# Optimization experiments

Measured on AMD Instinct MI355X. Metric: run time of the kernel, lower is better.

The kernel has to match this reference:

```python
import jax, jax.numpy as jnp
import numpy as np

B, S, D, H, O = 64, 512, 1024, 1024, 1024

def setup_inputs() -> dict:
    key = jax.random.key(0)
    k1, k2, k3 = jax.random.split(key, 3)
    x = jax.random.normal(k1, (B, S, D), dtype=jnp.float32)
    Wg = jax.random.normal(k2, (D + H, 3 * H), dtype=jnp.float32) / np.sqrt(D + H)
    bg = jnp.zeros((3 * H,), dtype=jnp.float32)
    Wc = jax.random.normal(k3, (H, O), dtype=jnp.float32) / np.sqrt(H)
    bc = jnp.zeros((O,), dtype=jnp.float32)
    return {"x": x, "Wg": Wg, "bg": bg, "Wc": Wc, "bc": bc}

def reference(x, Wg, bg, Wc, bc):
    # GRU cell matching the torch module: network = Linear(D+H, 3H)
    def step(h, x_t):
        combined = jnp.concatenate([x_t, h], axis=1)            # [B, D+H]
        gates = combined @ Wg + bg                              # [B, 3H]
        r_g, z_g, n_g = jnp.split(gates, 3, axis=1)
        r = jax.nn.sigmoid(r_g)
        z = jax.nn.sigmoid(z_g)
        n = jnp.tanh(n_g + r * h)
        h_next = (1 - z) * n + z * h
        return h_next, h_next

    h0 = jnp.zeros((x.shape[0], Wc.shape[0]), dtype=x.dtype)
    xs = jnp.swapaxes(x, 0, 1)                                  # [S, B, D]
    _, hs = jax.lax.scan(step, h0, xs)                          # hs: [S, B, H]
    outputs = jnp.swapaxes(hs, 0, 1)                            # [B, S, H]
    return outputs @ Wc + bc                                    # [B, S, O]
```

## Files before the change

### kernel.cpp

```cpp
#include <hip/hip_runtime.h>
#include <hip/hip_bf16.h>
#include <stdint.h>

#define BB   64
#define SS   512
#define DD   1024
#define HH   1024
#define TH3  3072
#define TCH  32

using frag8 = __attribute__((ext_vector_type(8))) short;
using f32x4 = __attribute__((ext_vector_type(4))) float;

__device__ __forceinline__ void split_bf16(float v, short& hi, short& lo) {
    uint32_t u = __float_as_uint(v);
    uint32_t uh = u & 0xFFFF0000u;
    float fl = v - __uint_as_float(uh);
    hi = (short)(uh >> 16);
    lo = (short)(__float_as_uint(fl) >> 16);
}

__global__ __launch_bounds__(256) void prep_w(
    const float* __restrict__ Wg, short* __restrict__ Wt_hi,
    short* __restrict__ Wt_lo)
{
    int idx = blockIdx.x * 256 + threadIdx.x;
    int lane = idx & 63;
    int f = idx >> 6;
    int kt = f & 63;
    int fg = f >> 6;
    int g = fg % 3;
    int jb = fg / 3;
    int krow = kt * 32 + (lane >> 4) * 8;
    int col = g * HH + jb * 16 + (lane & 15);
    size_t dst = (size_t)f * 512 + (size_t)lane * 8;
#pragma unroll
    for (int j = 0; j < 8; ++j) {
        float v = Wg[(size_t)(krow + j) * TH3 + col];
        short hi, lo;
        split_bf16(v, hi, lo);
        Wt_hi[dst + j] = hi;
        Wt_lo[dst + j] = lo;
    }
}

__global__ __launch_bounds__(256) void prep_wc(
    const float* __restrict__ Wc, short* __restrict__ Wct_hi,
    short* __restrict__ Wct_lo)
{
    int idx = blockIdx.x * 256 + threadIdx.x;
    int lane = idx & 63;
    int f = idx >> 6;
    int kt = f & 31;
    int jb = f >> 5;
    int krow = kt * 32 + (lane >> 4) * 8;
    int col = jb * 16 + (lane & 15);
    size_t dst = (size_t)f * 512 + (size_t)lane * 8;
#pragma unroll
    for (int j = 0; j < 8; ++j) {
        float v = Wc[(size_t)(krow + j) * HH + col];
        short hi, lo;
        split_bf16(v, hi, lo);
        Wct_hi[dst + j] = hi;
        Wct_lo[dst + j] = lo;
    }
}

__global__ __launch_bounds__(256) void gx_gemm(
    const short* __restrict__ Wt_hi, const short* __restrict__ Wt_lo,
    const float* __restrict__ x,
    const float* __restrict__ bg,
    float* __restrict__ gx,
    int t0)
{
    const int tid = threadIdx.x;
    const int lane = tid & 63;
    const int w = tid >> 6;
    const int jbg = blockIdx.x & 15;
    const int tl = blockIdx.x >> 4;
    const int t = t0 + tl;
    const int m0 = (w & 1) * 32;
    const int jbb = jbg * 4 + (w >> 1) * 2;
    const int kq = (lane >> 4) * 8;

    f32x4 acc[2][2][3];
#pragma unroll
    for (int mi = 0; mi < 2; ++mi)
#pragma unroll
        for (int jp = 0; jp < 2; ++jp)
#pragma unroll
            for (int g = 0; g < 3; ++g)
                acc[mi][jp][g] = (f32x4){0.f, 0.f, 0.f, 0.f};

    const float* xr0 = x + ((size_t)(m0 + (lane & 15)) * SS + t) * DD;
    const float* xr1 = xr0 + (size_t)16 * SS * DD;

    for (int kt = 0; kt < 32; ++kt) {
        frag8 ah[2], al[2];
#pragma unroll
        for (int mi = 0; mi < 2; ++mi) {
            const float* xp = (mi == 0 ? xr0 : xr1) + kt * 32 + kq;
            float xv[8];
            *(float4*)&xv[0] = *(const float4*)xp;
            *(float4*)&xv[4] = *(const float4*)(xp + 4);
#pragma unroll
            for (int j = 0; j < 8; ++j) {
                short hi, lo;
                split_bf16(xv[j], hi, lo);
                ah[mi][j] = hi;
                al[mi][j] = lo;
            }
        }
#pragma unroll
        for (int jp = 0; jp < 2; ++jp) {
#pragma unroll
            for (int g = 0; g < 3; ++g) {
                size_t base =
                    (((size_t)(jbb + jp) * 3 + g) * 64 + kt) * 512 + (size_t)lane * 8;
                frag8 bh = *(const frag8*)(Wt_hi + base);
                frag8 bl = *(const frag8*)(Wt_lo + base);
#pragma unroll
                for (int mi = 0; mi < 2; ++mi) {
                    f32x4 a = acc[mi][jp][g];
                    a = __builtin_amdgcn_mfma_f32_16x16x32_bf16(ah[mi], bh, a, 0, 0, 0);
                    a = __builtin_amdgcn_mfma_f32_16x16x32_bf16(ah[mi], bl, a, 0, 0, 0);
                    a = __builtin_amdgcn_mfma_f32_16x16x32_bf16(al[mi], bh, a, 0, 0, 0);
                    acc[mi][jp][g] = a;
                }
            }
        }
    }

    const int lcol = lane & 15;
    const int rq = (lane >> 4) * 4;
#pragma unroll
    for (int jp = 0; jp < 2; ++jp) {
        const int col = (jbb + jp) * 16 + lcol;
#pragma unroll
        for (int g = 0; g < 3; ++g) {
            const float bias = bg[g * HH + col];
#pragma unroll
            for (int mi = 0; mi < 2; ++mi) {
#pragma unroll
                for (int reg = 0; reg < 4; ++reg) {
                    int m = m0 + mi * 16 + rq + reg;
                    gx[((size_t)tl * BB + m) * TH3 + g * HH + col] =
                        acc[mi][jp][g][reg] + bias;
                }
            }
        }
    }
}

__global__ __launch_bounds__(256) void gru_step_h(
    const short* __restrict__ Wt_hi, const short* __restrict__ Wt_lo,
    const float* __restrict__ gx,
    const float* __restrict__ h_f,
    const short* __restrict__ h_hi,
    const short* __restrict__ h_lo,
    float* __restrict__ hn_f,
    short* __restrict__ hn_hi, short* __restrict__ hn_lo,
    __hip_bfloat16* __restrict__ hs,
    int t, int tl)
{
    __shared__ float red[12][256];

    const int tid = threadIdx.x;
    const int lane = tid & 63;
    const int w = tid >> 6;
    const int jb = blockIdx.x & 63;
    const int mt = blockIdx.x >> 6;
    const int m0 = mt * 16;
    const int mrow = m0 + (lane & 15);
    const int kq = (lane >> 4) * 8;

    const int lv = tid >> 2;
    const int reg = tid & 3;
    const int ecol = jb * 16 + (lv & 15);
    const int em = m0 + ((lv >> 4) << 2) + reg;
    const float* gp = gx + ((size_t)tl * BB + em) * TH3 + ecol;
    const float gxr = gp[0];
    const float gxz = gp[HH];
    const float gxn = gp[2 * HH];
    const float hold = h_f[(size_t)em * HH + ecol];

    f32x4 accr = {0.f, 0.f, 0.f, 0.f};
    f32x4 accz = {0.f, 0.f, 0.f, 0.f};
    f32x4 accn = {0.f, 0.f, 0.f, 0.f};
    const size_t fbase = (size_t)jb * 3 * 64;
    const short* hrh = h_hi + (size_t)mrow * HH;
    const short* hrl = h_lo + (size_t)mrow * HH;

#pragma unroll
    for (int i = 0; i < 8; ++i) {
        const int kt = w * 8 + i;
        frag8 a_hi = *(const frag8*)(hrh + kt * 32 + kq);
        frag8 a_lo = *(const frag8*)(hrl + kt * 32 + kq);
#pragma unroll
        for (int g = 0; g < 3; ++g) {
            size_t base = (fbase + (size_t)g * 64 + 32 + kt) * 512 + (size_t)lane * 8;
            frag8 b_hi = *(const frag8*)(Wt_hi + base);
            frag8 b_lo = *(const frag8*)(Wt_lo + base);
            f32x4 acc = (g == 0) ? accr : (g == 1) ? accz : accn;
            acc = __builtin_amdgcn_mfma_f32_16x16x32_bf16(a_hi, b_hi, acc, 0, 0, 0);
            acc = __builtin_amdgcn_mfma_f32_16x16x32_bf16(a_hi, b_lo, acc, 0, 0, 0);
            acc = __builtin_amdgcn_mfma_f32_16x16x32_bf16(a_lo, b_hi, acc, 0, 0, 0);
            if (g == 0) accr = acc; else if (g == 1) accz = acc; else accn = acc;
        }
    }

    *(f32x4*)&red[w * 3 + 0][lane * 4] = accr;
    *(f32x4*)&red[w * 3 + 1][lane * 4] = accz;
    *(f32x4*)&red[w * 3 + 2][lane * 4] = accn;
    __syncthreads();

    float rg = gxr + red[0][tid] + red[3][tid] + red[6][tid] + red[9][tid];
    float zg = gxz + red[1][tid] + red[4][tid] + red[7][tid] + red[10][tid];
    float ng = gxn + red[2][tid] + red[5][tid] + red[8][tid] + red[11][tid];

    float r = 1.f / (1.f + __expf(-rg));
    float z = 1.f / (1.f + __expf(-zg));
    float na = ng + r * hold;
    float n = 1.f - 2.f / (1.f + __expf(2.f * na));
    float hn = (1.f - z) * n + z * hold;

    hn_f[(size_t)em * HH + ecol] = hn;
    short hi, lo;
    split_bf16(hn, hi, lo);
    hn_hi[(size_t)em * HH + ecol] = hi;
    hn_lo[(size_t)em * HH + ecol] = lo;
    hs[((size_t)em * SS + t) * HH + ecol] = __float2bfloat16(hn);
}

__global__ __launch_bounds__(256) void out_mfma(
    const short* __restrict__ Wct_hi, const short* __restrict__ Wct_lo,
    const __hip_bfloat16* __restrict__ hs,
    const float* __restrict__ bc, float* __restrict__ out)
{
    const int tid = threadIdx.x;
    const int lane = tid & 63;
    const int w = tid >> 6;
    const int nb = blockIdx.x & 7;
    const int mb = blockIdx.x >> 3;
    const int r0 = mb * 128 + (w & 1) * 64;
    const int jb0 = nb * 8 + (w >> 1) * 4;
    const int kq = (lane >> 4) * 8;

    f32x4 acc[4][4];
#pragma unroll
    for (int i = 0; i < 4; ++i)
#pragma unroll
        for (int j = 0; j < 4; ++j) acc[i][j] = (f32x4){0.f, 0.f, 0.f, 0.f};

    const short* ar[4];
#pragma unroll
    for (int i = 0; i < 4; ++i)
        ar[i] = (const short*)hs +
                (size_t)(r0 + i * 16 + (lane & 15)) * HH + kq;

    for (int kt = 0; kt < 32; ++kt) {
        frag8 a[4];
#pragma unroll
        for (int i = 0; i < 4; ++i)
            a[i] = *(const frag8*)(ar[i] + kt * 32);
#pragma unroll
        for (int j = 0; j < 4; ++j) {
            size_t base = ((size_t)(jb0 + j) * 32 + kt) * 512 + (size_t)lane * 8;
            frag8 bh = *(const frag8*)(Wct_hi + base);
            frag8 bl = *(const frag8*)(Wct_lo + base);
#pragma unroll
            for (int i = 0; i < 4; ++i) {
                acc[i][j] = __builtin_amdgcn_mfma_f32_16x16x32_bf16(a[i], bh, acc[i][j], 0, 0, 0);
                acc[i][j] = __builtin_amdgcn_mfma_f32_16x16x32_bf16(a[i], bl, acc[i][j], 0, 0, 0);
            }
        }
    }

    const int lcol = lane & 15;
    const int rq = (lane >> 4) * 4;
#pragma unroll
    for (int j = 0; j < 4; ++j) {
        const int col = (jb0 + j) * 16 + lcol;
        const float bias = bc[col];
#pragma unroll
        for (int i = 0; i < 4; ++i) {
#pragma unroll
            for (int reg = 0; reg < 4; ++reg) {
                int row = r0 + i * 16 + rq + reg;
                out[(size_t)row * HH + col] = acc[i][j][reg] + bias;
            }
        }
    }
}

extern "C" void kernel_launch(void* const* d_in, const int* in_sizes, int n_in,
                              void* d_out, int out_size, void* d_ws, size_t ws_size,
                              hipStream_t stream) {
    const float* x  = (const float*)d_in[0];
    const float* Wg = (const float*)d_in[1];
    const float* bg = (const float*)d_in[2];
    const float* Wc = (const float*)d_in[3];
    const float* bc = (const float*)d_in[4];
    float* out = (float*)d_out;

    char* ws = (char*)d_ws;
    __hip_bfloat16* hs = (__hip_bfloat16*)ws;
    short* Wt_hi = (short*)(ws + 67108864);
    short* Wt_lo = (short*)(ws + 67108864 + 12582912);
    char* state = ws + 67108864 + 2 * 12582912;
    const size_t SET = 524288;
    float* gx = (float*)(state + 2 * SET);
    short* Wct_hi = (short*)gx;
    short* Wct_lo = Wct_hi + 1048576;

    float* hf[2];  short* hhi[2]; short* hlo[2];
    for (int p = 0; p < 2; ++p) {
        hf[p]  = (float*)(state + p * SET);
        hhi[p] = (short*)(state + p * SET + 262144);
        hlo[p] = (short*)(state + p * SET + 393216);
    }

    hipMemsetAsync(state, 0, SET, stream);

    prep_w<<<3072, 256, 0, stream>>>(Wg, Wt_hi, Wt_lo);

    for (int t0 = 0; t0 < SS; t0 += TCH) {
        gx_gemm<<<512, 256, 0, stream>>>(Wt_hi, Wt_lo, x, bg, gx, t0);
        for (int tl = 0; tl < TCH; ++tl) {
            int t = t0 + tl;
            int c = t & 1, n = c ^ 1;
            gru_step_h<<<256, 256, 0, stream>>>(
                Wt_hi, Wt_lo, gx,
                hf[c], hhi[c], hlo[c],
                hf[n], hhi[n], hlo[n],
                hs, t, tl);
        }
    }

    {
        prep_wc<<<512, 256, 0, stream>>>(Wc, Wct_hi, Wct_lo);
        out_mfma<<<2048, 256, 0, stream>>>(Wct_hi, Wct_lo, hs, bc, out);
    }
}
```

Measured before the change: 5.518 ms.

## Fuse per-timestep GRU launches into persistent cooperative kernel with register-resident weights

Replaces 32 per-timestep kernel launches per chunk with one cooperative persistent kernel that loops over the chunk's timesteps. Blocks in the same batch tile synchronize through an atomic counter with acquire/release spin waits instead of kernel boundaries. Each block also loads its slice of the recurrent weights into registers once, using 512 threads (8 waves) so each wave holds a smaller K slice. This removes launch overhead and repeated weight fetches, at the cost of spin-wait latency, high register pressure, and reliance on all 256 blocks being co-resident.

After: 12.48 ms. 126% more time.

```diff
diff --git a/kernel.cpp b/kernel.cpp
--- a/kernel.cpp
+++ b/kernel.cpp
@@ -11,6 +11,8 @@
 
 using frag8 = __attribute__((ext_vector_type(8))) short;
 using f32x4 = __attribute__((ext_vector_type(4))) float;
+
+#define MFMA_BF16(a, b, c) __builtin_amdgcn_mfma_f32_16x16x32_bf16(a, b, c, 0, 0, 0)
 
 __device__ __forceinline__ void split_bf16(float v, short& hi, short& lo) {
     uint32_t u = __float_as_uint(v);
@@ -122,9 +124,9 @@
 #pragma unroll
                 for (int mi = 0; mi < 2; ++mi) {
                     f32x4 a = acc[mi][jp][g];
-                    a = __builtin_amdgcn_mfma_f32_16x16x32_bf16(ah[mi], bh, a, 0, 0, 0);
-                    a = __builtin_amdgcn_mfma_f32_16x16x32_bf16(ah[mi], bl, a, 0, 0, 0);
-                    a = __builtin_amdgcn_mfma_f32_16x16x32_bf16(al[mi], bh, a, 0, 0, 0);
+                    a = MFMA_BF16(ah[mi], bh, a);
+                    a = MFMA_BF16(ah[mi], bl, a);
+                    a = MFMA_BF16(al[mi], bh, a);
                     acc[mi][jp][g] = a;
                 }
             }
@@ -152,18 +154,16 @@
     }
 }
 
-__global__ __launch_bounds__(256) void gru_step_h(
+__global__ __launch_bounds__(512, 2) void gru_seg(
     const short* __restrict__ Wt_hi, const short* __restrict__ Wt_lo,
     const float* __restrict__ gx,
-    const float* __restrict__ h_f,
-    const short* __restrict__ h_hi,
-    const short* __restrict__ h_lo,
-    float* __restrict__ hn_f,
-    short* __restrict__ hn_hi, short* __restrict__ hn_lo,
+    float* __restrict__ h0f, short* __restrict__ h0hi, short* __restrict__ h0lo,
+    float* __restrict__ h1f, short* __restrict__ h1hi, short* __restrict__ h1lo,
     __hip_bfloat16* __restrict__ hs,
-    int t, int tl)
-{
-    __shared__ float red[12][256];
+    int* __restrict__ cnt,
+    int t0)
+{
+    __shared__ float red[24][256];
 
     const int tid = threadIdx.x;
     const int lane = tid & 63;
@@ -171,65 +171,109 @@
     const int jb = blockIdx.x & 63;
     const int mt = blockIdx.x >> 6;
     const int m0 = mt * 16;
+    const int kq = (lane >> 4) * 8;
     const int mrow = m0 + (lane & 15);
-    const int kq = (lane >> 4) * 8;
+    const size_t rowoff = (size_t)mrow * HH;
+
+    frag8 bh[3][4], bl[3][4];
+    {
+        const size_t fbase = (size_t)jb * 3 * 64;
+#pragma unroll
+        for (int g = 0; g < 3; ++g)
+#pragma unroll
+            for (int i = 0; i < 4; ++i) {
+                size_t base = (fbase + (size_t)g * 64 + 32 + (w * 4 + i)) * 512
+                              + (size_t)lane * 8;
+                bh[g][i] = *(const frag8*)(Wt_hi + base);
+                bl[g][i] = *(const frag8*)(Wt_lo + base);
+            }
+    }
 
     const int lv = tid >> 2;
     const int reg = tid & 3;
     const int ecol = jb * 16 + (lv & 15);
     const int em = m0 + ((lv >> 4) << 2) + reg;
-    const float* gp = gx + ((size_t)tl * BB + em) * TH3 + ecol;
-    const float gxr = gp[0];
-    const float gxz = gp[HH];
-    const float gxn = gp[2 * HH];
-    const float hold = h_f[(size_t)em * HH + ecol];
-
-    f32x4 accr = {0.f, 0.f, 0.f, 0.f};
-    f32x4 accz = {0.f, 0.f, 0.f, 0.f};
-    f32x4 accn = {0.f, 0.f, 0.f, 0.f};
-    const size_t fbase = (size_t)jb * 3 * 64;
-    const short* hrh = h_hi + (size_t)mrow * HH;
-    const short* hrl = h_lo + (size_t)mrow * HH;
-
-#pragma unroll
-    for (int i = 0; i < 8; ++i) {
-        const int kt = w * 8 + i;
-        frag8 a_hi = *(const frag8*)(hrh + kt * 32 + kq);
-        frag8 a_lo = *(const frag8*)(hrl + kt * 32 + kq);
-#pragma unroll
-        for (int g = 0; g < 3; ++g) {
-            size_t base = (fbase + (size_t)g * 64 + 32 + kt) * 512 + (size_t)lane * 8;
-            frag8 b_hi = *(const frag8*)(Wt_hi + base);
-            frag8 b_lo = *(const frag8*)(Wt_lo + base);
-            f32x4 acc = (g == 0) ? accr : (g == 1) ? accz : accn;
-            acc = __builtin_amdgcn_mfma_f32_16x16x32_bf16(a_hi, b_hi, acc, 0, 0, 0);
-            acc = __builtin_amdgcn_mfma_f32_16x16x32_bf16(a_hi, b_lo, acc, 0, 0, 0);
-            acc = __builtin_amdgcn_mfma_f32_16x16x32_bf16(a_lo, b_hi, acc, 0, 0, 0);
-            if (g == 0) accr = acc; else if (g == 1) accz = acc; else accn = acc;
-        }
-    }
-
-    *(f32x4*)&red[w * 3 + 0][lane * 4] = accr;
-    *(f32x4*)&red[w * 3 + 1][lane * 4] = accz;
-    *(f32x4*)&red[w * 3 + 2][lane * 4] = accn;
-    __syncthreads();
-
-    float rg = gxr + red[0][tid] + red[3][tid] + red[6][tid] + red[9][tid];
-    float zg = gxz + red[1][tid] + red[4][tid] + red[7][tid] + red[10][tid];
-    float ng = gxn + red[2][tid] + red[5][tid] + red[8][tid] + red[11][tid];
-
-    float r = 1.f / (1.f + __expf(-rg));
-    float z = 1.f / (1.f + __expf(-zg));
-    float na = ng + r * hold;
-    float n = 1.f - 2.f / (1.f + __expf(2.f * na));
-    float hn = (1.f - z) * n + z * hold;
-
-    hn_f[(size_t)em * HH + ecol] = hn;
-    short hi, lo;
-    split_bf16(hn, hi, lo);
-    hn_hi[(size_t)em * HH + ecol] = hi;
-    hn_lo[(size_t)em * HH + ecol] = lo;
-    hs[((size_t)em * SS + t) * HH + ecol] = __float2bfloat16(hn);
+    const size_t eoff = (size_t)em * HH + ecol;
+    int* cnt_mt = cnt + mt * 32;
+
+    for (int tl = 0; tl < TCH; ++tl) {
+        const int t = t0 + tl;
+        const int cur = tl & 1;
+        const short* hrh = (cur ? h1hi : h0hi) + rowoff;
+        const short* hrl = (cur ? h1lo : h0lo) + rowoff;
+
+        float gxr = 0.f, gxz = 0.f, gxnn = 0.f, hold = 0.f;
+        if (tid < 256) {
+            const float* gp = gx + ((size_t)tl * BB + em) * TH3 + ecol;
+            gxr = gp[0];
+            gxz = gp[HH];
+            gxnn = gp[2 * HH];
+            hold = (cur ? h1f : h0f)[eoff];
+        }
+
+        frag8 ah[4], al[4];
+#pragma unroll
+        for (int i = 0; i < 4; ++i) {
+            const int kt = w * 4 + i;
+            ah[i] = *(const frag8*)(hrh + kt * 32 + kq);
+            al[i] = *(const frag8*)(hrl + kt * 32 + kq);
+        }
+
+        f32x4 accr = {0.f, 0.f, 0.f, 0.f};
+        f32x4 accz = {0.f, 0.f, 0.f, 0.f};
+        f32x4 accn = {0.f, 0.f, 0.f, 0.f};
+#pragma unroll
+        for (int i = 0; i < 4; ++i) {
+            accr = MFMA_BF16(ah[i], bh[0][i], accr);
+            accr = MFMA_BF16(ah[i], bl[0][i], accr);
+            accr = MFMA_BF16(al[i], bh[0][i], accr);
+            accz = MFMA_BF16(ah[i], bh[1][i], accz);
+            accz = MFMA_BF16(ah[i], bl[1][i], accz);
+            accz = MFMA_BF16(al[i], bh[1][i], accz);
+            accn = MFMA_BF16(ah[i], bh[2][i], accn);
+            accn = MFMA_BF16(ah[i], bl[2][i], accn);
+            accn = MFMA_BF16(al[i], bh[2][i], accn);
+        }
+
+        *(f32x4*)&red[w * 3 + 0][lane * 4] = accr;
+        *(f32x4*)&red[w * 3 + 1][lane * 4] = accz;
+        *(f32x4*)&red[w * 3 + 2][lane * 4] = accn;
+        __syncthreads();
+
+        if (tid < 256) {
+            float rg = gxr, zg = gxz, ng = gxnn;
+#pragma unroll
+            for (int ww = 0; ww < 8; ++ww) {
+                rg += red[ww * 3 + 0][tid];
+                zg += red[ww * 3 + 1][tid];
+                ng += red[ww * 3 + 2][tid];
+            }
+            float r = 1.f / (1.f + __expf(-rg));
+            float z = 1.f / (1.f + __expf(-zg));
+            float na = ng + r * hold;
+            float n = 1.f - 2.f / (1.f + __expf(2.f * na));
+            float hn = (1.f - z) * n + z * hold;
+
+            (cur ? h0f : h1f)[eoff] = hn;
+            short hi, lo;
+            split_bf16(hn, hi, lo);
+            (cur ? h0hi : h1hi)[eoff] = hi;
+            (cur ? h0lo : h1lo)[eoff] = lo;
+            hs[((size_t)em * SS + t) * HH + ecol] = __float2bfloat16(hn);
+        }
+        __syncthreads();
+
+        if (tid == 0) {
+            __threadfence();
+            __hip_atomic_fetch_add(cnt_mt, 1, __ATOMIC_RELEASE,
+                                   __HIP_MEMORY_SCOPE_AGENT);
+            const int target = 64 * (t + 1);
+            while (__hip_atomic_load(cnt_mt, __ATOMIC_ACQUIRE,
+                                     __HIP_MEMORY_SCOPE_AGENT) < target)
+                __builtin_amdgcn_s_sleep(1);
+        }
+        __syncthreads();
+    }
 }
 
 __global__ __launch_bounds__(256) void out_mfma(
@@ -266,12 +310,12 @@
 #pragma unroll
         for (int j = 0; j < 4; ++j) {
             size_t base = ((size_t)(jb0 + j) * 32 + kt) * 512 + (size_t)lane * 8;
-            frag8 bh = *(const frag8*)(Wct_hi + base);
-            frag8 bl = *(const frag8*)(Wct_lo + base);
+            frag8 bhf = *(const frag8*)(Wct_hi + base);
+            frag8 blf = *(const frag8*)(Wct_lo + base);
 #pragma unroll
             for (int i = 0; i < 4; ++i) {
-                acc[i][j] = __builtin_amdgcn_mfma_f32_16x16x32_bf16(a[i], bh, acc[i][j], 0, 0, 0);
-                acc[i][j] = __builtin_amdgcn_mfma_f32_16x16x32_bf16(a[i], bl, acc[i][j], 0, 0, 0);
+                acc[i][j] = MFMA_BF16(a[i], bhf, acc[i][j]);
+                acc[i][j] = MFMA_BF16(a[i], blf, acc[i][j]);
             }
         }
     }
@@ -310,6 +354,7 @@
     char* state = ws + 67108864 + 2 * 12582912;
     const size_t SET = 524288;
     float* gx = (float*)(state + 2 * SET);
+    int* cnt = (int*)(state + 2 * SET + 25165824);
     short* Wct_hi = (short*)gx;
     short* Wct_lo = Wct_hi + 1048576;
 
@@ -321,19 +366,25 @@
     }
 
     hipMemsetAsync(state, 0, SET, stream);
+    hipMemsetAsync(cnt, 0, 512, stream);
 
     prep_w<<<3072, 256, 0, stream>>>(Wg, Wt_hi, Wt_lo);
 
     for (int t0 = 0; t0 < SS; t0 += TCH) {
         gx_gemm<<<512, 256, 0, stream>>>(Wt_hi, Wt_lo, x, bg, gx, t0);
-        for (int tl = 0; tl < TCH; ++tl) {
-            int t = t0 + tl;
-            int c = t & 1, n = c ^ 1;
-            gru_step_h<<<256, 256, 0, stream>>>(
-                Wt_hi, Wt_lo, gx,
-                hf[c], hhi[c], hlo[c],
-                hf[n], hhi[n], hlo[n],
-                hs, t, tl);
+
+        const short* a0 = Wt_hi; const short* a1 = Wt_lo;
+        const float* a2 = gx;
+        float* a3 = hf[0]; short* a4 = hhi[0]; short* a5 = hlo[0];
+        float* a6 = hf[1]; short* a7 = hhi[1]; short* a8 = hlo[1];
+        __hip_bfloat16* a9 = hs; int* a10 = cnt; int a11 = t0;
+        void* args[] = {&a0, &a1, &a2, &a3, &a4, &a5, &a6, &a7, &a8,
+                        &a9, &a10, &a11};
+        hipError_t ce = hipLaunchCooperativeKernel(
+            gru_seg, dim3(256), dim3(512), args, 0, stream);
+        if (ce != hipSuccess) {
+            gru_seg<<<dim3(256), dim3(512), 0, stream>>>(
+                a0, a1, a2, a3, a4, a5, a6, a7, a8, a9, a10, a11);
         }
     }
 
```
